# Optimization experiments

Measured on AMD Instinct MI355X. Metric: run time of the kernel, lower is better.

Reference implementation:

```python
import jax, jax.numpy as jnp
from jax import lax
import numpy as np

NF = 64      # feature channels
G = 8        # mask groups
NBR = 3      # top-k neighbors
PATCH = 7    # correlation patch size (patches[0])
CORK = 3     # correlation / unfold kernel size
PAD_COR = 1  # (CORK-1)//2
PAD_S = 4    # PAD_COR + (PATCH-1)//2
ADD = 6      # 2*PAD_S - CORK + 1
B, H, W = 4, 96, 96


def leaky(x):
    return jnp.where(x >= 0, x, 0.1 * x)


def _conv(x, w, b, pad):
    y = lax.conv_general_dilated(x, w, (1, 1), [(pad[0], pad[0]), (pad[1], pad[1])],
                                 dimension_numbers=('NCHW', 'OIHW', 'NCHW'))
    return y + b[None, :, None, None]


def _normalize(x, eps=1e-12):
    n = jnp.sqrt(jnp.sum(x * x, axis=1, keepdims=True))
    return x / jnp.maximum(n, eps)


def _correlation(f1, f2):
    # spatial-correlation-sampler: kernel=3, patch=7, stride=1, pad=1, dilations=1
    # out[b, ph*7+pw, i, j] = sum_{c,u,v} f1p[b,c,i+u,j+v] * f2p[b,c,i+u+ph-3, j+v+pw-3]
    # (unnormalized; only topk indices are consumed downstream, so any positive
    #  constant scale is irrelevant)
    Bx, C, Hx, Wx = f1.shape
    f1p = jnp.pad(f1, ((0, 0), (0, 0), (PAD_COR, PAD_COR), (PAD_COR, PAD_COR)))
    f2p = jnp.pad(f2, ((0, 0), (0, 0), (PAD_S, PAD_S), (PAD_S, PAD_S)))
    outs = []
    for ph in range(PATCH):
        for pw in range(PATCH):
            s = jnp.sum(f1p * f2p[:, :, ph:ph + Hx + 2, pw:pw + Wx + 2], axis=1)  # [B,H+2,W+2]
            o = sum(s[:, u:u + Hx, v:v + Wx] for u in range(CORK) for v in range(CORK))
            outs.append(o)
    return jnp.stack(outs, axis=1)  # [B, 49, H, W]


def setup_inputs() -> dict:
    key = jax.random.key(0)
    ks = jax.random.split(key, 16)

    def wt(k, shape):
        fan_in = shape[1] * shape[2] * shape[3]
        return jax.random.normal(k, shape, jnp.float32) * (1.0 / np.sqrt(fan_in))

    return {
        'ref_fea_l': jax.random.normal(ks[0], (B, NF, H, W), jnp.float32),
        'w1': wt(ks[1], (NF, NF * 2, 3, 3)), 'b1': jnp.zeros((NF,), jnp.float32),
        'w2': wt(ks[2], (NF, NF, 3, 3)),     'b2': jnp.zeros((NF,), jnp.float32),
        'w3': wt(ks[3], (NF, NF, 7, 1)),     'b3': jnp.zeros((NF,), jnp.float32),
        'w4': wt(ks[4], (NF, NF, 1, 7)),     'b4': jnp.zeros((NF,), jnp.float32),
        'wm': wt(ks[5], (G * CORK ** 2, NF, 3, 3)), 'bm': jnp.zeros((G * CORK ** 2,), jnp.float32),
        'wnn': wt(ks[6], (NF, NF * NBR, 3, 3)), 'bnn': jnp.zeros((NF,), jnp.float32),
        'wf': wt(ks[7], (NF, NF * 2, 3, 3)),    'bf': jnp.zeros((NF,), jnp.float32),
    }


def reference(ref_fea_l, w1, b1, w2, b2, w3, b3, w4, b4, wm, bm, wnn, bnn, wf, bf):
    Bx, C, Hx, Wx = ref_fea_l.shape
    nbr_fea = ref_fea_l  # aliased in the original forward

    # mask branch
    x = jnp.concatenate([nbr_fea, ref_fea_l], axis=1)
    x = leaky(_conv(x, w1, b1, (1, 1)))
    x = leaky(_conv(x, w2, b2, (1, 1)))
    x = leaky(_conv(x, w3, b3, (3, 0)))
    x = leaky(_conv(x, w4, b4, (0, 3)))
    mask = _conv(x, wm, bm, (1, 1)).reshape(Bx, G, 1, CORK ** 2, Hx, Wx)

    # correlation + topk neighbor displacements
    nref = _normalize(ref_fea_l)
    corr = _correlation(nref, nref)                     # [B,49,H,W]
    _, idx = lax.top_k(corr.transpose(0, 2, 3, 1), NBR)  # [B,H,W,NBR]

    # flat indices into the (H+6)x(W+6) unfold grid
    ph = idx // PATCH
    pw = idx % PATCH
    yy = jnp.arange(Hx)[:, None, None]
    xx = jnp.arange(Wx)[None, :, None]
    flat = ((ph + yy) * (Wx + ADD) + (pw + xx)).reshape(Bx, Hx * Wx * NBR)

    # unfold (im2col) of nbr features with pad 4, then gather chosen 3x3 patches
    nbr_pad = jnp.pad(nbr_fea, ((0, 0), (0, 0), (PAD_S, PAD_S), (PAD_S, PAD_S)))
    patches = lax.conv_general_dilated_patches(nbr_pad, (CORK, CORK), (1, 1), 'VALID',
                                               dimension_numbers=('NCHW', 'OIHW', 'NCHW'))
    pl = patches.reshape(Bx, C * CORK ** 2, -1).transpose(0, 2, 1)  # [B, (H+6)(W+6), C*9]
    gath = jnp.take_along_axis(pl, flat[:, :, None], axis=1)        # [B, HW*NBR, C*9]
    gath = gath.reshape(Bx * Hx * Wx, NBR * C, CORK, CORK)

    # conv over gathered patches then modulated mask-weighted reduce
    g = leaky(_conv(gath, wnn, bnn, (1, 1)))                         # [BHW, C, 3, 3]
    g = g.reshape(Bx, Hx, Wx, C, CORK ** 2).transpose(0, 3, 4, 1, 2)
    g = g.reshape(Bx, G, C // G, CORK ** 2, Hx, Wx)
    agg = leaky(jnp.sum(g * mask, axis=3).reshape(Bx, C, Hx, Wx))

    out = leaky(_conv(jnp.concatenate([ref_fea_l, agg], axis=1), wf, bf, (1, 1)))
    return out
```

## Files before the change

### kernel.cpp

```cpp
#include <hip/hip_runtime.h>
#include <hip/hip_bf16.h>

constexpr int BATCH = 4;
constexpr int H = 96, W = 96, HW = H * W;
constexpr int NBR = 3;

using bf16x8 = __attribute__((ext_vector_type(8))) short;
using f32x4 = __attribute__((ext_vector_type(4))) float;

static __device__ __forceinline__ float leakyf(float x) {
    return x >= 0.f ? x : 0.1f * x;
}

static __device__ __forceinline__ short f2bf(float x) {
    __hip_bfloat16 h = __float2bfloat16(x);
    return *reinterpret_cast<short*>(&h);
}

static __device__ __forceinline__ float bf2f(short s) {
    __hip_bfloat16 h = *reinterpret_cast<__hip_bfloat16*>(&s);
    return __bfloat162float(h);
}

__global__ __launch_bounds__(256) void k_pre(const float* __restrict__ ref,
                                             short* __restrict__ reft,
                                             float* __restrict__ nrn) {
    int p = blockIdx.x * 256 + threadIdx.x;
    if (p >= BATCH * HW) return;
    int b = p / HW, ij = p % HW;
    const float* src = ref + b * 64 * HW + ij;
    float v[64];
    float ss = 0.f;
#pragma unroll
    for (int c = 0; c < 64; ++c) {
        v[c] = src[c * HW];
        ss += v[c] * v[c];
    }
    float inv = 1.f / fmaxf(sqrtf(ss), 1e-12f);
    short* rd = reft + (size_t)p * 64;
#pragma unroll
    for (int cc = 0; cc < 8; ++cc) {
        bf16x8 o;
#pragma unroll
        for (int j = 0; j < 8; ++j) o[j] = f2bf(v[cc * 8 + j]);
        *(bf16x8*)(rd + cc * 8) = o;
    }
    float* nd = nrn + b * 64 * HW + ij;
#pragma unroll
    for (int c = 0; c < 64; ++c) nd[c * HW] = v[c] * inv;
}

static __device__ __forceinline__ void packw(const float* __restrict__ src,
                                             short* __restrict__ dst, int i,
                                             int OC, int ICt, int ICsrc, int KH,
                                             int KW, int NT, int fold) {
    int e = i & 7, l = (i >> 3) & 63;
    int rest = i >> 9;
    int nt = rest % NT;
    rest /= NT;
    int ICK = ICt >> 5;
    int kk = rest % ICK;
    int tap = rest / ICK;
    int ic = kk * 32 + (l >> 4) * 8 + e;
    int oc = nt * 16 + (l & 15);
    int u = tap / KW, v = tap % KW;
    float val = 0.f;
    if (oc < OC) {
        val = src[((oc * ICsrc + ic) * KH + u) * KW + v];
        if (fold) val += src[((oc * ICsrc + 64 + ic) * KH + u) * KW + v];
    }
    dst[i] = f2bf(val);
}

constexpr int E1 = 36864, E2 = 36864, E3 = 28672, E4 = 28672, E5 = 46080,
              E6 = 73728, E7 = 110592;
constexpr int C1 = E1, C2 = C1 + E2, C3 = C2 + E3, C4 = C3 + E4, C5 = C4 + E5,
              C6 = C5 + E6, C7 = C6 + E7, CT = C7 + 8;
__global__ void k_prep_all(const float* __restrict__ w1,
                           const float* __restrict__ w2,
                           const float* __restrict__ w3,
                           const float* __restrict__ w4,
                           const float* __restrict__ wm,
                           const float* __restrict__ wf,
                           const float* __restrict__ wnn,
                           short* __restrict__ P1, short* __restrict__ P2,
                           short* __restrict__ P3, short* __restrict__ P4,
                           short* __restrict__ PM, short* __restrict__ PF,
                           short* __restrict__ B2, short* __restrict__ zpad) {
    int i = blockIdx.x * 256 + threadIdx.x;
    if (i >= CT) return;
    if (i < C1) {
        packw(w1, P1, i, 64, 64, 128, 3, 3, 4, 1);
    } else if (i < C2) {
        packw(w2, P2, i - C1, 64, 64, 64, 3, 3, 4, 0);
    } else if (i < C3) {
        packw(w3, P3, i - C2, 64, 64, 64, 7, 1, 4, 0);
    } else if (i < C4) {
        packw(w4, P4, i - C3, 64, 64, 64, 1, 7, 4, 0);
    } else if (i < C5) {
        packw(wm, PM, i - C4, 72, 64, 64, 3, 3, 5, 0);
    } else if (i < C6) {
        packw(wf, PF, i - C5, 64, 128, 128, 3, 3, 4, 0);
    } else if (i < C7) {
        int j = i - C6;
        int e = j & 7, l = (j >> 3) & 63;
        int t = (j >> 9) % 9;
        int h2 = (j / (512 * 9)) % 2;
        int n = (j / (512 * 9 * 2)) % 3;
        int nt = j / (512 * 9 * 2 * 3);
        int oc = nt * 16 + (l & 15);
        int c = h2 * 32 + (l >> 4) * 8 + e;
        int u = t / 3, v = t % 3;
        B2[j] = f2bf(wnn[((oc * 192 + n * 64 + c) * 3 + u) * 3 + v]);
    } else {
        zpad[i - C7] = 0;
    }
}

static __device__ void corr2_body(const float* __restrict__ nr,
                                  float* __restrict__ S, int blk) {
    int idx = blk * 256 + threadIdx.x;
    if (idx >= BATCH * 49 * 98 * 49) return;
    int xp = idx % 49, x0 = xp * 2, x1 = x0 + 1;
    int y = (idx / 49) % 98;
    int d = (idx / (49 * 98)) % 49;
    int b = idx / (49 * 98 * 49);
    int dy = d / 7, dx = d % 7;
    float* row = S + ((size_t)(b * 49 + d)) * (98 * 98) + y * 98;
    if (d > 24) {
        int yy = y + dy - 3;
        if (yy < 0 || yy >= 98) {
            row[x0] = 0.f;
            row[x1] = 0.f;
        } else {
            if (x0 + dx - 3 < 0 || x0 + dx - 3 >= 98) row[x0] = 0.f;
            if (x1 + dx - 3 < 0 || x1 + dx - 3 >= 98) row[x1] = 0.f;
        }
        return;
    }
    int f1i = y - 1, f2i = y + dy - 4;
    float r0 = 0.f, r1 = 0.f;
    if (f1i >= 0 && f1i < H && f2i >= 0 && f2i < H) {
        int f1j0 = x0 - 1, f2j0 = x0 + dx - 4;
        bool v0 = f1j0 >= 0 && f1j0 < W && f2j0 >= 0 && f2j0 < W;
        bool v1 = f1j0 + 1 >= 0 && f1j0 + 1 < W && f2j0 + 1 >= 0 && f2j0 + 1 < W;
        const float* p1 = nr + (size_t)b * 64 * HW + f1i * W + f1j0;
        const float* p2 = nr + (size_t)b * 64 * HW + f2i * W + f2j0;
        if (v0 && v1) {
#pragma unroll 16
            for (int c = 0; c < 64; ++c) {
                float2 a = *(const float2*)(p1 + c * HW);
                float2 q = *(const float2*)(p2 + c * HW);
                r0 = fmaf(a.x, q.x, r0);
                r1 = fmaf(a.y, q.y, r1);
            }
        } else {
            if (v0) {
#pragma unroll 16
                for (int c = 0; c < 64; ++c) r0 = fmaf(p1[c * HW], p2[c * HW], r0);
            }
            if (v1) {
#pragma unroll 16
                for (int c = 0; c < 64; ++c)
                    r1 = fmaf(p1[1 + c * HW], p2[1 + c * HW], r1);
            }
        }
    }
    row[x0] = r0;
    row[x1] = r1;
    if (d < 24) {
        int y2 = y + dy - 3;
        if (y2 >= 0 && y2 < 98) {
            float* mrow = S + ((size_t)(b * 49 + 48 - d)) * (98 * 98) + y2 * 98;
            int x20 = x0 + dx - 3;
            if (x20 >= 0 && x20 < 98) mrow[x20] = r0;
            if (x20 + 1 >= 0 && x20 + 1 < 98) mrow[x20 + 1] = r1;
        }
    }
}

static __device__ void topk_body(const float* __restrict__ S,
                                 int* __restrict__ idx3, int blk) {
    int p = blk * 256 + threadIdx.x;
    if (p >= BATCH * HW) return;
    int b = p / HW, i = (p % HW) / W, j = p % W;
    float v0 = -1e30f, v1 = -1e30f, v2 = -1e30f;
    int d0 = 0, d1 = 0, d2 = 0;
    for (int d = 0; d < 49; ++d) {
        const float* s = S + ((b * 49 + d) * 98 + i) * 98 + j;
        float v = 0.f;
#pragma unroll
        for (int u = 0; u < 3; ++u)
#pragma unroll
            for (int vv = 0; vv < 3; ++vv) v += s[u * 98 + vv];
        if (v > v0) {
            v2 = v1; d2 = d1; v1 = v0; d1 = d0; v0 = v; d0 = d;
        } else if (v > v1) {
            v2 = v1; d2 = d1; v1 = v; d1 = d;
        } else if (v > v2) {
            v2 = v; d2 = d;
        }
    }
    idx3[p * 3 + 0] = d0;
    idx3[p * 3 + 1] = d1;
    idx3[p * 3 + 2] = d2;
}

template <int KH, int KW, int IC, int OC, int OMODE, bool BLDS, int NSPL, int TAIL>
__global__ __launch_bounds__(256) void k_cmfma(
    const short* __restrict__ inA, const short* __restrict__ inB,
    const short* __restrict__ Bp, const float* __restrict__ bias,
    void* __restrict__ outp, const float* __restrict__ taux,
    float* __restrict__ tS, int* __restrict__ tidx, int convblks) {
    if (TAIL != 0 && (int)blockIdx.x >= convblks) {
        int xb = (int)blockIdx.x - convblks;
        if (TAIL == 1)
            corr2_body(taux, tS, xb);
        else
            topk_body(taux, tidx, xb);
        return;
    }
    constexpr int TI = 8, TJ = 16;
    constexpr int PH = (KH - 1) / 2, PW = (KW - 1) / 2;
    constexpr int LR = TI + KH - 1, LC = TJ + KW - 1;
    constexpr int ICB = IC * 2;
    constexpr int LS = (ICB == 128) ? 7 : 8;
    constexpr int ICK = IC / 32;
    constexpr int NTF = (OC + 15) / 16;
    constexpr int NTb = NTF / NSPL;
    constexpr int TAPS = KH * KW;
    constexpr int NOCT = ICB / 16;
    __shared__ char Xs[LR * LC * ICB];
    __shared__ short Bs[BLDS ? TAPS * ICK * NTb * 512 : 8];
    const int lid = blockIdx.x;
    const int tj0 = (lid % 6) * TJ, ti0 = ((lid / 6) % 12) * TI;
    const int zz = lid / 72;
    const int b = zz / NSPL;
    const int nt0 = (zz % NSPL) * NTb;
    const int tid = threadIdx.x;
    if (BLDS) {
        for (int u2 = tid; u2 < TAPS * ICK * NTb * 64; u2 += 256) {
            int l2 = u2 & 63;
            int rest = u2 >> 6;
            int nt = rest % NTb;
            int qk = rest / NTb;
            ((bf16x8*)Bs)[u2] = ((const bf16x8*)Bp)[(qk * NTF + nt0 + nt) * 64 + l2];
        }
    }
    for (int u2 = tid; u2 < LR * LC * NOCT; u2 += 256) {
        int oct = u2 % NOCT;
        int hp = u2 / NOCT;
        int hr = hp / LC, hc = hp % LC;
        int gi = ti0 + hr - PH, gj = tj0 + hc - PW;
        bf16x8 v = {};
        if (gi >= 0 && gi < H && gj >= 0 && gj < W) {
            const short* s = (oct < 8) ? inA : inB;
            v = *(const bf16x8*)(s + (size_t)(b * HW + gi * W + gj) * 64 +
                                 (oct & 7) * 8);
        }
        int byte = hp * ICB + oct * 16;
        byte ^= ((byte >> LS) & 7) << 4;
        *(bf16x8*)(Xs + byte) = v;
    }
    __syncthreads();
    const int wave = tid >> 6, l = tid & 63;
    const int r = l & 15, q = l >> 4;
    const int mt0 = wave * 2;
    int p0 = mt0 * 16 + r, p1 = p0 + 16;
    int li0 = p0 >> 4, lj0 = p0 & 15, li1 = p1 >> 4, lj1 = p1 & 15;
    f32x4 acc[2][NTb] = {};
#pragma unroll
    for (int t = 0; t < TAPS; ++t) {
        const int u = t / KW, v = t % KW;
        int hp0 = (li0 + u) * LC + (lj0 + v);
        int hp1 = (li1 + u) * LC + (lj1 + v);
#pragma unroll
        for (int kk = 0; kk < ICK; ++kk) {
            int ab0 = hp0 * ICB + kk * 64 + q * 16;
            ab0 ^= ((ab0 >> LS) & 7) << 4;
            int ab1 = hp1 * ICB + kk * 64 + q * 16;
            ab1 ^= ((ab1 >> LS) & 7) << 4;
            bf16x8 a0 = *(const bf16x8*)(Xs + ab0);
            bf16x8 a1 = *(const bf16x8*)(Xs + ab1);
            const short* bbase =
                BLDS ? (const short*)Bs + (t * ICK + kk) * NTb * 512 + l * 8
                     : Bp + ((t * ICK + kk) * NTF + nt0) * 512 + l * 8;
#pragma unroll
            for (int nt = 0; nt < NTb; ++nt) {
                bf16x8 bv = *(const bf16x8*)(bbase + nt * 512);
                acc[0][nt] =
                    __builtin_amdgcn_mfma_f32_16x16x32_bf16(a0, bv, acc[0][nt], 0, 0, 0);
                acc[1][nt] =
                    __builtin_amdgcn_mfma_f32_16x16x32_bf16(a1, bv, acc[1][nt], 0, 0, 0);
            }
        }
    }
    const int col = l & 15;
#pragma unroll
    for (int mt = 0; mt < 2; ++mt)
#pragma unroll
        for (int nt = 0; nt < NTb; ++nt) {
            int oc = (nt0 + nt) * 16 + col;
            float bs = (oc < OC) ? bias[oc] : 0.f;
#pragma unroll
            for (int j = 0; j < 4; ++j) {
                int p = (mt0 + mt) * 16 + q * 4 + j;
                int gi = ti0 + (p >> 4), gj = tj0 + (p & 15);
                float val = acc[mt][nt][j] + bs;
                if (OMODE == 0) {
                    val = leakyf(val);
                    *((short*)outp + (size_t)(b * HW + gi * W + gj) * 64 + oc) =
                        f2bf(val);
                } else if (OMODE == 1) {
                    if (oc < 72)
                        *((short*)outp + (size_t)(b * HW + gi * W + gj) * 72 + oc) =
                            f2bf(val);
                } else {
                    val = leakyf(val);
                    *((float*)outp + (size_t)(b * 64 + oc) * HW + gi * W + gj) = val;
                }
            }
        }
}

__global__ __launch_bounds__(512, 4) void k_agg_mfma(
    const short* __restrict__ refT, const int* __restrict__ idx3,
    const short* __restrict__ B2, const float* __restrict__ bnn,
    const short* __restrict__ maskT, const short* __restrict__ zpad,
    short* __restrict__ agg) {
    constexpr int PX = 32;
    constexpr int BUFB = 36864;
    __shared__ short A_lds[2 * 2 * 18 * 64 * 8];
    __shared__ short sgi[PX][NBR], sgj[PX][NBR];
    const int bid = blockIdx.x;
    const int swz = (bid & 7) * ((int)gridDim.x >> 3) + (bid >> 3);
    const int p0 = swz * PX;
    const int b = p0 / HW;
    const int i0 = (p0 % HW) / W;
    const int j0 = p0 % W;
    const int tid = threadIdx.x;
    const int wave = tid >> 6;
    const int lane = tid & 63;
    if (tid < PX * NBR) {
        int px = tid / NBR, n = tid % NBR;
        int d = idx3[(p0 + px) * NBR + n];
        sgi[px][n] = (short)(i0 + d / 7 - 4);
        sgj[px][n] = (short)(j0 + px + d % 7 - 4);
    }
    __syncthreads();

    auto STAGE = [&](int n, int buf) {
        for (int r2 = wave; r2 < 36; r2 += 8) {
            int kkl = r2 % 18;
            int ph = r2 / 18;
            int rs = kkl >> 1;
            int oh = kkl & 1;
            int c = lane ^ (((lane >> 4) & 3) | (((buf * 36 + r2) & 1) << 2));
            int oct = oh * 4 + (c >> 4);
            int px = ph * 16 + (c & 15);
            int gi = sgi[px][n] + rs / 3;
            int gj = sgj[px][n] + rs % 3;
            const short* src = (gi >= 0 && gi < H && gj >= 0 && gj < W)
                                   ? refT + (size_t)(b * HW + gi * W + gj) * 64 +
                                         oct * 8
                                   : zpad;
            __builtin_amdgcn_global_load_lds(
                (const __attribute__((address_space(1))) void*)src,
                (__attribute__((address_space(3))) void*)((char*)A_lds +
                                                          buf * BUFB + r2 * 1024),
                16, 0, 0);
        }
    };

    const int w = wave & 3;
    const int half = wave >> 2;
    f32x4 acc[9] = {};
    const short* Bw = B2 + (size_t)w * (3 * 2 * 9 * 512) + lane * 8;

    auto COMPUTE = [&](int n, int buf) {
#pragma unroll
        for (int h2 = 0; h2 < 2; ++h2) {
            const short* bb = Bw + (n * 2 + h2) * 9 * 512;
            bf16x8 bv[9];
#pragma unroll
            for (int t = 0; t < 9; ++t) bv[t] = *(const bf16x8*)(bb + t * 512);
#pragma unroll
            for (int rs = 0; rs < 9; ++rs) {
                int kkl = rs * 2 + h2;
                int ab = buf * BUFB + ((((half * 18 + kkl) << 6) + lane) << 4);
                ab ^= ((ab >> 8) & 7) << 4;
                bf16x8 a = *(const bf16x8*)((char*)A_lds + ab);
#pragma unroll
                for (int t = 0; t < 9; ++t) {
                    const int y = rs / 3 - t / 3 + 1;
                    const int x = rs % 3 - t % 3 + 1;
                    if (y >= 0 && y < 3 && x >= 0 && x < 3)
                        acc[y * 3 + x] = __builtin_amdgcn_mfma_f32_16x16x32_bf16(
                            a, bv[t], acc[y * 3 + x], 0, 0, 0);
                }
            }
        }
    };

    STAGE(0, 0);
    STAGE(1, 1);
    __syncthreads();
    COMPUTE(0, 0);
    __syncthreads();
    STAGE(2, 0);
    COMPUTE(1, 1);
    __syncthreads();
    COMPUTE(2, 0);

    const int oc = w * 16 + (lane & 15);
    const float bn = bnn[oc];
    const int mrow = (lane >> 4) * 4;
#pragma unroll
    for (int j = 0; j < 4; ++j) {
        int px = half * 16 + mrow + j;
        int ij = i0 * W + j0 + px;
        const short* mb = maskT + (size_t)(b * HW + ij) * 72 + (oc >> 3) * 9;
        float sacc = 0.f;
#pragma unroll
        for (int yx = 0; yx < 9; ++yx) {
            float gv = leakyf(acc[yx][j] + bn);
            sacc += gv * bf2f(mb[yx]);
        }
        agg[(size_t)(b * HW + ij) * 64 + oc] = f2bf(leakyf(sacc));
    }
}

extern "C" void kernel_launch(void* const* d_in, const int* in_sizes, int n_in,
                              void* d_out, int out_size, void* d_ws,
                              size_t ws_size, hipStream_t stream) {
    const float* ref = (const float*)d_in[0];
    const float* w1 = (const float*)d_in[1];
    const float* b1 = (const float*)d_in[2];
    const float* w2 = (const float*)d_in[3];
    const float* b2 = (const float*)d_in[4];
    const float* w3 = (const float*)d_in[5];
    const float* b3 = (const float*)d_in[6];
    const float* w4 = (const float*)d_in[7];
    const float* b4 = (const float*)d_in[8];
    const float* wm = (const float*)d_in[9];
    const float* bm = (const float*)d_in[10];
    const float* wnn = (const float*)d_in[11];
    const float* bnn = (const float*)d_in[12];
    const float* wf = (const float*)d_in[13];
    const float* bf = (const float*)d_in[14];

    char* ws = (char*)d_ws;
    constexpr size_t O_NRN = 0;
    constexpr size_t O_S = O_NRN + (size_t)BATCH * HW * 64 * 4;
    constexpr size_t O_REFT = O_S + (size_t)BATCH * 49 * 98 * 98 * 4;
    constexpr size_t O_X1 = O_REFT + (size_t)BATCH * HW * 64 * 2;
    constexpr size_t O_X2 = O_X1 + (size_t)BATCH * HW * 64 * 2;
    constexpr size_t O_MASKT = O_X2 + (size_t)BATCH * HW * 64 * 2;
    constexpr size_t O_IDX = O_MASKT + (size_t)BATCH * HW * 72 * 2;
    constexpr size_t O_P1 = O_IDX + (size_t)BATCH * HW * 3 * 4;
    constexpr size_t O_P2 = O_P1 + (size_t)E1 * 2;
    constexpr size_t O_P3 = O_P2 + (size_t)E2 * 2;
    constexpr size_t O_P4 = O_P3 + (size_t)E3 * 2;
    constexpr size_t O_PM = O_P4 + (size_t)E4 * 2;
    constexpr size_t O_PF = O_PM + (size_t)E5 * 2;
    constexpr size_t O_B2 = O_PF + (size_t)E6 * 2;
    constexpr size_t O_ZP = O_B2 + (size_t)E7 * 2;

    float* NRN = (float*)(ws + O_NRN);
    float* S = (float*)(ws + O_S);
    short* REFT = (short*)(ws + O_REFT);
    short* X1 = (short*)(ws + O_X1);
    short* X2 = (short*)(ws + O_X2);
    short* MASKT = (short*)(ws + O_MASKT);
    int* IDX = (int*)(ws + O_IDX);
    short* P1 = (short*)(ws + O_P1);
    short* P2 = (short*)(ws + O_P2);
    short* P3 = (short*)(ws + O_P3);
    short* P4 = (short*)(ws + O_P4);
    short* PM = (short*)(ws + O_PM);
    short* PF = (short*)(ws + O_PF);
    short* B2 = (short*)(ws + O_B2);
    short* ZPAD = (short*)(ws + O_ZP);

    constexpr int CONVB = 6 * 12 * BATCH * 4;
    constexpr int CORRB = (BATCH * 49 * 98 * 49 + 255) / 256;
    constexpr int TOPKB = BATCH * HW / 256;

    k_pre<<<(BATCH * HW + 255) / 256, 256, 0, stream>>>(ref, REFT, NRN);
    k_prep_all<<<(CT + 255) / 256, 256, 0, stream>>>(w1, w2, w3, w4, wm, wf, wnn,
                                                     P1, P2, P3, P4, PM, PF, B2,
                                                     ZPAD);

    k_cmfma<3, 3, 64, 64, 0, true, 4, 1><<<CONVB + CORRB, 256, 0, stream>>>(
        REFT, nullptr, P1, b1, X1, NRN, S, nullptr, CONVB);
    k_cmfma<3, 3, 64, 64, 0, true, 4, 2><<<CONVB + TOPKB, 256, 0, stream>>>(
        X1, nullptr, P2, b2, X2, S, nullptr, IDX, CONVB);
    k_cmfma<7, 1, 64, 64, 0, true, 4, 0><<<CONVB, 256, 0, stream>>>(
        X2, nullptr, P3, b3, X1, nullptr, nullptr, nullptr, CONVB);
    k_cmfma<1, 7, 64, 64, 0, true, 4, 0><<<CONVB, 256, 0, stream>>>(
        X1, nullptr, P4, b4, X2, nullptr, nullptr, nullptr, CONVB);
    k_cmfma<3, 3, 64, 72, 1, true, 5, 0><<<6 * 12 * BATCH * 5, 256, 0, stream>>>(
        X2, nullptr, PM, bm, MASKT, nullptr, nullptr, nullptr, 6 * 12 * BATCH * 5);

    k_agg_mfma<<<BATCH * HW / 32, 512, 0, stream>>>(REFT, IDX, B2, bnn, MASKT,
                                                    ZPAD, X1);

    k_cmfma<3, 3, 128, 64, 2, false, 2, 0><<<6 * 12 * BATCH * 2, 256, 0, stream>>>(
        REFT, X1, PF, bf, d_out, nullptr, nullptr, nullptr, 6 * 12 * BATCH * 2);
}
```

Measured before the change: 203.6 us.

## Tile correlation through LDS with channel-last normalized features and separate zero fill

The normalized features are now written channel-last instead of channel-planar. The correlation tail is rewritten so each block handles two output rows: it stages f1 and f2 rows for 8 channels at a time in shared memory, and each thread accumulates all 25 displacements in registers. This replaces the old one-thread-per-pair scheme that re-read every channel from global memory. Zero-filling of the out-of-bounds mirrored displacement entries moves to a separate kernel, and the conv kernel's shared memory becomes a pool shared with the correlation tail. The trade-offs are an extra launch, more shared memory and register pressure, and scattered mirrored stores.

```diff
diff --git a/kernel.cpp b/kernel.cpp
--- a/kernel.cpp
+++ b/kernel.cpp
@@ -24,7 +24,7 @@
 
 __global__ __launch_bounds__(256) void k_pre(const float* __restrict__ ref,
                                              short* __restrict__ reft,
-                                             float* __restrict__ nrn) {
+                                             float* __restrict__ nrt) {
     int p = blockIdx.x * 256 + threadIdx.x;
     if (p >= BATCH * HW) return;
     int b = p / HW, ij = p % HW;
@@ -45,9 +45,9 @@
         for (int j = 0; j < 8; ++j) o[j] = f2bf(v[cc * 8 + j]);
         *(bf16x8*)(rd + cc * 8) = o;
     }
-    float* nd = nrn + b * 64 * HW + ij;
-#pragma unroll
-    for (int c = 0; c < 64; ++c) nd[c * HW] = v[c] * inv;
+    float* nd = nrt + (size_t)p * 64;
+#pragma unroll
+    for (int c = 0; c < 64; ++c) nd[c] = v[c] * inv;
 }
 
 static __device__ __forceinline__ void packw(const float* __restrict__ src,
@@ -117,64 +117,91 @@
     }
 }
 
-static __device__ void corr2_body(const float* __restrict__ nr,
-                                  float* __restrict__ S, int blk) {
-    int idx = blk * 256 + threadIdx.x;
-    if (idx >= BATCH * 49 * 98 * 49) return;
+__global__ void k_zfill(float* __restrict__ S) {
+    int idx = blockIdx.x * 256 + threadIdx.x;
+    if (idx >= BATCH * 24 * 98 * 49) return;
     int xp = idx % 49, x0 = xp * 2, x1 = x0 + 1;
     int y = (idx / 49) % 98;
-    int d = (idx / (49 * 98)) % 49;
-    int b = idx / (49 * 98 * 49);
+    int dd = (idx / (49 * 98)) % 24;
+    int b = idx / (49 * 98 * 24);
+    int d = 25 + dd;
     int dy = d / 7, dx = d % 7;
     float* row = S + ((size_t)(b * 49 + d)) * (98 * 98) + y * 98;
-    if (d > 24) {
-        int yy = y + dy - 3;
-        if (yy < 0 || yy >= 98) {
-            row[x0] = 0.f;
-            row[x1] = 0.f;
-        } else {
-            if (x0 + dx - 3 < 0 || x0 + dx - 3 >= 98) row[x0] = 0.f;
-            if (x1 + dx - 3 < 0 || x1 + dx - 3 >= 98) row[x1] = 0.f;
-        }
-        return;
-    }
-    int f1i = y - 1, f2i = y + dy - 4;
-    float r0 = 0.f, r1 = 0.f;
-    if (f1i >= 0 && f1i < H && f2i >= 0 && f2i < H) {
-        int f1j0 = x0 - 1, f2j0 = x0 + dx - 4;
-        bool v0 = f1j0 >= 0 && f1j0 < W && f2j0 >= 0 && f2j0 < W;
-        bool v1 = f1j0 + 1 >= 0 && f1j0 + 1 < W && f2j0 + 1 >= 0 && f2j0 + 1 < W;
-        const float* p1 = nr + (size_t)b * 64 * HW + f1i * W + f1j0;
-        const float* p2 = nr + (size_t)b * 64 * HW + f2i * W + f2j0;
-        if (v0 && v1) {
-#pragma unroll 16
-            for (int c = 0; c < 64; ++c) {
-                float2 a = *(const float2*)(p1 + c * HW);
-                float2 q = *(const float2*)(p2 + c * HW);
-                r0 = fmaf(a.x, q.x, r0);
-                r1 = fmaf(a.y, q.y, r1);
+    int yy = y + dy - 3;
+    if (yy < 0 || yy >= 98) {
+        row[x0] = 0.f;
+        row[x1] = 0.f;
+    } else {
+        if (x0 + dx - 3 < 0 || x0 + dx - 3 >= 98) row[x0] = 0.f;
+        if (x1 + dx - 3 < 0 || x1 + dx - 3 >= 98) row[x1] = 0.f;
+    }
+}
+
+constexpr int CORR_NCOL = 104;
+constexpr int CORR_BYTES = (2 * 5 * CORR_NCOL + 2 * 2 * CORR_NCOL) * 16;
+static __device__ void corr_tile_body(const float* __restrict__ nrt,
+                                      float* __restrict__ S, char* pool,
+                                      int blk) {
+    float4* f2s = (float4*)pool;
+    float4* f1s = f2s + 2 * 5 * CORR_NCOL;
+    const int b = blk / 49;
+    const int y0 = (blk % 49) * 2;
+    const int tid = threadIdx.x;
+    const int x = tid % 98, yloc = tid / 98;
+    const int y = y0 + yloc;
+    float acc[25];
+#pragma unroll
+    for (int d = 0; d < 25; ++d) acc[d] = 0.f;
+    for (int c0 = 0; c0 < 64; c0 += 8) {
+        for (int e = tid; e < 2 * 5 * CORR_NCOL; e += 256) {
+            int sc = e % CORR_NCOL;
+            int r = (e / CORR_NCOL) % 5;
+            int g = e / (CORR_NCOL * 5);
+            int iy = y0 - 4 + r, ix = sc - 4;
+            float4 v = make_float4(0.f, 0.f, 0.f, 0.f);
+            if (iy >= 0 && iy < H && ix >= 0 && ix < W)
+                v = *(const float4*)(nrt + ((size_t)(b * HW) + iy * W + ix) * 64 +
+                                     c0 + g * 4);
+            f2s[(g * 5 + r) * CORR_NCOL + sc] = v;
+        }
+        for (int e = tid; e < 2 * 2 * CORR_NCOL; e += 256) {
+            int sc = e % CORR_NCOL;
+            int r = (e / CORR_NCOL) % 2;
+            int g = e / (CORR_NCOL * 2);
+            int iy = y0 - 1 + r, ix = sc - 4;
+            float4 v = make_float4(0.f, 0.f, 0.f, 0.f);
+            if (iy >= 0 && iy < H && ix >= 0 && ix < W)
+                v = *(const float4*)(nrt + ((size_t)(b * HW) + iy * W + ix) * 64 +
+                                     c0 + g * 4);
+            f1s[(g * 2 + r) * CORR_NCOL + sc] = v;
+        }
+        __syncthreads();
+        if (tid < 196) {
+#pragma unroll
+            for (int g = 0; g < 2; ++g) {
+                float4 a = f1s[(g * 2 + yloc) * CORR_NCOL + (x + 3)];
+#pragma unroll
+                for (int d = 0; d < 25; ++d) {
+                    const int dy = d / 7, dx = d % 7;
+                    float4 q = f2s[(g * 5 + yloc + dy) * CORR_NCOL + (x + dx)];
+                    acc[d] = fmaf(a.x, q.x,
+                                  fmaf(a.y, q.y,
+                                       fmaf(a.z, q.z, fmaf(a.w, q.w, acc[d]))));
+                }
             }
-        } else {
-            if (v0) {
-#pragma unroll 16
-                for (int c = 0; c < 64; ++c) r0 = fmaf(p1[c * HW], p2[c * HW], r0);
-            }
-            if (v1) {
-#pragma unroll 16
-                for (int c = 0; c < 64; ++c)
-                    r1 = fmaf(p1[1 + c * HW], p2[1 + c * HW], r1);
-            }
-        }
-    }
-    row[x0] = r0;
-    row[x1] = r1;
-    if (d < 24) {
-        int y2 = y + dy - 3;
-        if (y2 >= 0 && y2 < 98) {
-            float* mrow = S + ((size_t)(b * 49 + 48 - d)) * (98 * 98) + y2 * 98;
-            int x20 = x0 + dx - 3;
-            if (x20 >= 0 && x20 < 98) mrow[x20] = r0;
-            if (x20 + 1 >= 0 && x20 + 1 < 98) mrow[x20 + 1] = r1;
+        }
+        __syncthreads();
+    }
+    if (tid < 196) {
+#pragma unroll
+        for (int d = 0; d < 25; ++d)
+            S[((size_t)(b * 49 + d)) * (98 * 98) + y * 98 + x] = acc[d];
+#pragma unroll
+        for (int d = 0; d < 24; ++d) {
+            const int dy = d / 7, dx = d % 7;
+            int y2 = y + dy - 3, x2 = x + dx - 3;
+            if (y2 >= 0 && y2 < 98 && x2 >= 0 && x2 < 98)
+                S[((size_t)(b * 49 + 48 - d)) * (98 * 98) + y2 * 98 + x2] = acc[d];
         }
     }
 }
@@ -212,14 +239,6 @@
     const short* __restrict__ Bp, const float* __restrict__ bias,
     void* __restrict__ outp, const float* __restrict__ taux,
     float* __restrict__ tS, int* __restrict__ tidx, int convblks) {
-    if (TAIL != 0 && (int)blockIdx.x >= convblks) {
-        int xb = (int)blockIdx.x - convblks;
-        if (TAIL == 1)
-            corr2_body(taux, tS, xb);
-        else
-            topk_body(taux, tidx, xb);
-        return;
-    }
     constexpr int TI = 8, TJ = 16;
     constexpr int PH = (KH - 1) / 2, PW = (KW - 1) / 2;
     constexpr int LR = TI + KH - 1, LC = TJ + KW - 1;
@@ -230,8 +249,22 @@
     constexpr int NTb = NTF / NSPL;
     constexpr int TAPS = KH * KW;
     constexpr int NOCT = ICB / 16;
-    __shared__ char Xs[LR * LC * ICB];
-    __shared__ short Bs[BLDS ? TAPS * ICK * NTb * 512 : 8];
+    constexpr int XS_BYTES = LR * LC * ICB;
+    constexpr int BS_BYTES = BLDS ? TAPS * ICK * NTb * 1024 : 16;
+    constexpr int CONV_BYTES = XS_BYTES + BS_BYTES;
+    constexpr int POOL =
+        (TAIL == 1 && CORR_BYTES > CONV_BYTES) ? CORR_BYTES : CONV_BYTES;
+    __shared__ __align__(16) char pool[POOL];
+    if (TAIL != 0 && (int)blockIdx.x >= convblks) {
+        int xb = (int)blockIdx.x - convblks;
+        if (TAIL == 1)
+            corr_tile_body(taux, tS, pool, xb);
+        else
+            topk_body(taux, tidx, xb);
+        return;
+    }
+    char* Xs = pool;
+    short* Bs = (short*)(pool + XS_BYTES);
     const int lid = blockIdx.x;
     const int tj0 = (lid % 6) * TJ, ti0 = ((lid / 6) % 12) * TI;
     const int zz = lid / 72;
@@ -450,8 +483,8 @@
     const float* bf = (const float*)d_in[14];
 
     char* ws = (char*)d_ws;
-    constexpr size_t O_NRN = 0;
-    constexpr size_t O_S = O_NRN + (size_t)BATCH * HW * 64 * 4;
+    constexpr size_t O_NRT = 0;
+    constexpr size_t O_S = O_NRT + (size_t)BATCH * HW * 64 * 4;
     constexpr size_t O_REFT = O_S + (size_t)BATCH * 49 * 98 * 98 * 4;
     constexpr size_t O_X1 = O_REFT + (size_t)BATCH * HW * 64 * 2;
     constexpr size_t O_X2 = O_X1 + (size_t)BATCH * HW * 64 * 2;
@@ -466,7 +499,7 @@
     constexpr size_t O_B2 = O_PF + (size_t)E6 * 2;
     constexpr size_t O_ZP = O_B2 + (size_t)E7 * 2;
 
-    float* NRN = (float*)(ws + O_NRN);
+    float* NRT = (float*)(ws + O_NRT);
     float* S = (float*)(ws + O_S);
     short* REFT = (short*)(ws + O_REFT);
     short* X1 = (short*)(ws + O_X1);
@@ -483,16 +516,18 @@
     short* ZPAD = (short*)(ws + O_ZP);
 
     constexpr int CONVB = 6 * 12 * BATCH * 4;
-    constexpr int CORRB = (BATCH * 49 * 98 * 49 + 255) / 256;
+    constexpr int CORRB = BATCH * 49;
     constexpr int TOPKB = BATCH * HW / 256;
-
-    k_pre<<<(BATCH * HW + 255) / 256, 256, 0, stream>>>(ref, REFT, NRN);
+    constexpr int ZFB = (BATCH * 24 * 98 * 49 + 255) / 256;
+
+    k_pre<<<(BATCH * HW + 255) / 256, 256, 0, stream>>>(ref, REFT, NRT);
     k_prep_all<<<(CT + 255) / 256, 256, 0, stream>>>(w1, w2, w3, w4, wm, wf, wnn,
                                                      P1, P2, P3, P4, PM, PF, B2,
                                                      ZPAD);
+    k_zfill<<<ZFB, 256, 0, stream>>>(S);
 
     k_cmfma<3, 3, 64, 64, 0, true, 4, 1><<<CONVB + CORRB, 256, 0, stream>>>(
-        REFT, nullptr, P1, b1, X1, NRN, S, nullptr, CONVB);
+        REFT, nullptr, P1, b1, X1, NRT, S, nullptr, CONVB);
     k_cmfma<3, 3, 64, 64, 0, true, 4, 2><<<CONVB + TOPKB, 256, 0, stream>>>(
         X1, nullptr, P2, b2, X2, S, nullptr, IDX, CONVB);
     k_cmfma<7, 1, 64, 64, 0, true, 4, 0><<<CONVB, 256, 0, stream>>>(
```

After: 182.7 us. -10.3%, faster.
